# Kernel tuning notes

Measured on AMD Instinct MI355X. Metric: run time of the kernel, lower is better.

The kernel has to match this reference:

```python
import jax, jax.numpy as jnp
import numpy as np

N_NODES = 100000
N_EDGES = 3200000
F = 32          # n_node_features
L = 50          # n_node_labels
EL = 10         # n_edge_labels
K = 16          # out_dim (graph_data.num_classes)


def setup_inputs() -> dict:
    key = jax.random.key(0)
    ks = jax.random.split(key, 12)
    x = jax.random.normal(ks[0], (N_NODES, F), dtype=jnp.float32)
    node_labels = jax.random.randint(ks[1], (N_NODES,), 0, L, dtype=jnp.int32)
    edge_src = jax.random.randint(ks[2], (N_EDGES,), 0, N_NODES, dtype=jnp.int32)
    edge_dst = jax.random.randint(ks[3], (N_EDGES,), 0, N_NODES, dtype=jnp.int32)
    edge_labels = jax.random.randint(ks[4], (N_EDGES,), 0, EL, dtype=jnp.int32)
    s = 0.1
    W1 = jax.random.normal(ks[5], (L, L, EL), dtype=jnp.float32) * s
    b1 = jax.random.normal(ks[6], (L,), dtype=jnp.float32) * s
    W2 = jax.random.normal(ks[7], (L, L, EL), dtype=jnp.float32) * s
    b2 = jax.random.normal(ks[8], (L,), dtype=jnp.float32) * s
    W3 = jax.random.normal(ks[9], (L, L, EL), dtype=jnp.float32) * s
    b3 = jax.random.normal(ks[10], (L,), dtype=jnp.float32) * s
    kr1, kr2 = jax.random.split(ks[11])
    Wr = jax.random.normal(kr1, (L, F, K), dtype=jnp.float32) * s
    br = jax.random.normal(kr2, (K,), dtype=jnp.float32) * s
    return {"x": x, "W1": W1, "b1": b1, "W2": W2, "b2": b2, "W3": W3, "b3": b3,
            "Wr": Wr, "br": br, "node_labels": node_labels,
            "edge_src": edge_src, "edge_dst": edge_dst, "edge_labels": edge_labels}


def _conv(x, W, b, node_labels, edge_src, edge_dst, edge_labels):
    # weight_rule_wf: per-edge scalar weight indexed by (src label, dst label, edge label)
    w_e = W[node_labels[edge_src], node_labels[edge_dst], edge_labels]  # [E]
    msgs = w_e[:, None] * x[edge_src]                                   # [E, F]
    agg = jax.ops.segment_sum(msgs, edge_dst, num_segments=x.shape[0])  # [N, F]
    # node_label_rule bias: per-node bias indexed by node label, then Tanh
    return jnp.tanh(agg + b[node_labels][:, None])


def reference(x, W1, b1, W2, b2, W3, b3, Wr, br,
              node_labels, edge_src, edge_dst, edge_labels):
    h = _conv(x, W1, b1, node_labels, edge_src, edge_dst, edge_labels)
    h = _conv(h, W2, b2, node_labels, edge_src, edge_dst, edge_labels)
    h = _conv(h, W3, b3, node_labels, edge_src, edge_dst, edge_labels)
    # GraphResizeLayer (node_label_rule): out[k] = sum_i Wr[label_i, f, k] * h[i, f] + br[k]
    # equivalent efficient form: pre-aggregate node features by label, then contract.
    sums = jax.ops.segment_sum(h, node_labels, num_segments=Wr.shape[0])  # [L, F]
    out = jnp.tanh(jnp.einsum('lf,lfk->k', sums, Wr) + br)                # [K]
    return out
```

## Files before the change

kernel.cpp:

```cpp
#include <hip/hip_runtime.h>
#include <hip/hip_bf16.h>
#include <hip/hip_fp16.h>
#include <hip/hip_fp8.h>

#define NN 100000
#define NE 3200000
#define FF 32
#define LL 50
#define ELB 10
#define KK 16
#define NWIDX (LL * LL * ELB)

#define CH 8192
#define NBLK_P1 391
#define NBUK 391
#define CAP 9216

typedef float floatx2 __attribute__((ext_vector_type(2)));

__device__ __forceinline__ float fast_tanh(float x) {
    float e = __expf(2.0f * x);
    return 1.0f - 2.0f / (e + 1.0f);
}

__global__ __launch_bounds__(512) void p1_scatter(const int* __restrict__ esrc,
                                                  const int* __restrict__ edst,
                                                  const int* __restrict__ elab,
                                                  const float* __restrict__ x,
                                                  const float* __restrict__ W1,
                                                  const float* __restrict__ W2,
                                                  const float* __restrict__ W3,
                                                  float4* __restrict__ Wi,
                                                  unsigned char* __restrict__ labels8,
                                                  const int* __restrict__ labels,
                                                  unsigned* __restrict__ xb,
                                                  int* __restrict__ cursor,
                                                  unsigned* __restrict__ recs) {
    __shared__ int lcnt[NBUK];
    __shared__ int lofs[NBUK];
    __shared__ int lbase[NBUK];
    __shared__ int sc[512];
    __shared__ unsigned srec[CH];
    __shared__ unsigned sgad[CH];
    int tid = threadIdx.x;
    for (int i = blockIdx.x * 512 + tid; i < NN * FF / 4; i += NBLK_P1 * 512) {
        float4 v = ((const float4*)x)[i];
        __hip_fp8_e4m3 a(v.x), b(v.y), c(v.z), d(v.w);
        xb[i] = (unsigned)a.__x | ((unsigned)b.__x << 8) |
                ((unsigned)c.__x << 16) | ((unsigned)d.__x << 24);
    }
    for (int i = blockIdx.x * 512 + tid; i < NWIDX; i += NBLK_P1 * 512)
        Wi[i] = make_float4(W1[i], W2[i], W3[i], 0.f);
    for (int i = blockIdx.x * 512 + tid; i < NN; i += NBLK_P1 * 512)
        labels8[i] = (unsigned char)labels[i];
    for (int i = tid; i < NBUK; i += 512) lcnt[i] = 0;
    __syncthreads();
    long e0 = (long)blockIdx.x * CH;
    long rem = NE - e0;
    int cnt = rem < CH ? (int)rem : CH;
    int nq = cnt >> 2;
    const int4* edst4 = (const int4*)(edst + e0);
    const int4* esrc4 = (const int4*)(esrc + e0);
    const int4* elab4 = (const int4*)(elab + e0);
    for (int i = tid; i < nq; i += 512) {
        int4 d = edst4[i];
        atomicAdd(&lcnt[d.x >> 8], 1);
        atomicAdd(&lcnt[d.y >> 8], 1);
        atomicAdd(&lcnt[d.z >> 8], 1);
        atomicAdd(&lcnt[d.w >> 8], 1);
    }
    __syncthreads();
    sc[tid] = (tid < NBUK) ? lcnt[tid] : 0;
    __syncthreads();
    for (int ofs = 1; ofs < 512; ofs <<= 1) {
        int t = (tid >= ofs) ? sc[tid - ofs] : 0;
        __syncthreads();
        sc[tid] += t;
        __syncthreads();
    }
    if (tid < NBUK) {
        int c = lcnt[tid];
        lofs[tid] = sc[tid] - c;
        lbase[tid] = c ? atomicAdd(&cursor[tid], c) : 0;
        lcnt[tid] = 0;
    }
    __syncthreads();
    for (int i = tid; i < nq; i += 512) {
        int4 s4 = esrc4[i];
        int4 l4 = elab4[i];
        int4 d4 = edst4[i];
#pragma unroll
        for (int k = 0; k < 4; ++k) {
            int s  = (&s4.x)[k];
            int d  = (&d4.x)[k];
            int el = (&l4.x)[k];
            int b = d >> 8;
            int pos = atomicAdd(&lcnt[b], 1);
            int slot = lofs[b] + pos;
            srec[slot] = ((unsigned)s << 12) | ((unsigned)el << 8) | (unsigned)(d & 255);
            int rel = lbase[b] + pos;
            sgad[slot] = (rel < CAP) ? (unsigned)(b * CAP + rel) : 0xFFFFFFFFu;
        }
    }
    __syncthreads();
    for (int i = tid; i < cnt; i += 512) {
        unsigned g = sgad[i];
        if (g != 0xFFFFFFFFu)
            recs[g] = srec[i];
    }
}

__global__ __launch_bounds__(512) void p2_local(const int* __restrict__ cursor,
                                                const unsigned* __restrict__ recs,
                                                const unsigned char* __restrict__ labels8,
                                                const float4* __restrict__ Wi,
                                                unsigned long long* __restrict__ ed,
                                                int* __restrict__ gstart,
                                                int* __restrict__ gcnt) {
    __shared__ int deg[256], loff[256], lcur[256], sc[256];
    __shared__ int labd[256];
    __shared__ unsigned pk32[CAP];
    int b = blockIdx.x, tid = threadIdx.x;
    int base = b * CAP;
    int n = cursor[b];
    if (n > CAP) n = CAP;
    if (tid < 256) {
        int node = (b << 8) + tid;
        deg[tid] = 0;
        lcur[tid] = 0;
        labd[tid] = (node < NN) ? (int)labels8[node] : 0;
    }
    __syncthreads();
    for (int i = tid; i < n; i += 512)
        atomicAdd(&deg[(int)(recs[base + i] & 255)], 1);
    __syncthreads();
    if (tid < 256) sc[tid] = deg[tid];
    __syncthreads();
    for (int ofs = 1; ofs < 256; ofs <<= 1) {
        int t = (tid >= ofs && tid < 256) ? sc[tid - ofs] : 0;
        __syncthreads();
        if (tid < 256) sc[tid] += t;
        __syncthreads();
    }
    if (tid < 256) {
        loff[tid] = sc[tid] - deg[tid];
        int node = (b << 8) + tid;
        if (node < NN) { gstart[node] = base + loff[tid]; gcnt[node] = deg[tid]; }
    }
    __syncthreads();
    for (int i = tid; i < n; i += 512) {
        unsigned r = recs[base + i];
        int dl  = (int)(r & 255);
        int el  = (int)((r >> 8) & 15);
        int src = (int)(r >> 12);
        int widx = (int)labels8[src] * (LL * ELB) + labd[dl] * ELB + el;
        int ofs = atomicAdd(&lcur[dl], 1);
        pk32[loff[dl] + ofs] = ((unsigned)widx << 17) | (unsigned)src;
    }
    __syncthreads();
    for (int slot = tid; slot < n; slot += 512) {
        unsigned v = pk32[slot];
        int widx = (int)(v >> 17);
        unsigned src = v & 0x1FFFFu;
        float4 wv = Wi[widx];
        unsigned long long h1 = __half_as_ushort(__float2half(wv.x));
        unsigned long long h2 = __half_as_ushort(__float2half(wv.y));
        unsigned long long h3 = __half_as_ushort(__float2half(wv.z)) >> 1;
        ed[base + slot] = h1 | (h2 << 16) | (h3 << 32)
                        | ((unsigned long long)src << 47);
    }
}

__global__ __launch_bounds__(256) void conv_kernel(const unsigned char* __restrict__ xin,
                                                   unsigned char* __restrict__ hout,
                                                   const int* __restrict__ gstart,
                                                   const int* __restrict__ gcnt,
                                                   const unsigned long long* __restrict__ ed,
                                                   const float* __restrict__ bias,
                                                   const int* __restrict__ labels,
                                                   const int wmode) {
    __shared__ unsigned stage[2][8][64];
    int tid = threadIdx.x;
    int hw = tid >> 5, lane = tid & 31;
    int node = (blockIdx.x << 3) + hw;
    int s = gstart[node];
    int n = gcnt[node];
    float bb = bias[labels[node]];
    int eg = lane >> 3;
    int fg = (lane & 7) << 2;
    float4 acc = {0.f, 0.f, 0.f, 0.f};
    unsigned long long e_cur = ed[s + (lane < n ? lane : 0)];
    int buf = 0;
    for (int base = 0; base < n; base += 32) {
        int idx = base + lane;
        float w = 0.f;
        unsigned so = 0u;
        if (idx < n) {
            unsigned short h;
            if (wmode == 0)      h = (unsigned short)e_cur;
            else if (wmode == 1) h = (unsigned short)(e_cur >> 16);
            else                 h = (unsigned short)(((e_cur >> 32) & 0x7FFFull) << 1);
            w = __half2float(__ushort_as_half(h));
            so = (unsigned)(e_cur >> 47) << 5;
        }
        ((uint2*)&stage[buf][hw][0])[lane] = make_uint2(__float_as_uint(w), so);
        int nb = base + 32;
        if (nb < n) {
            int i2 = nb + lane;
            e_cur = ed[s + (i2 < n ? i2 : nb)];
        }
        __builtin_amdgcn_wave_barrier();
#pragma unroll
        for (int j = 0; j < 8; ++j) {
            uint2 ws = ((const uint2*)&stage[buf][hw][0])[j * 4 + eg];
            unsigned pv = *(const unsigned*)(xin + ws.y + fg);
            floatx2 lo = __builtin_amdgcn_cvt_pk_f32_fp8((int)pv, false);
            floatx2 hi = __builtin_amdgcn_cvt_pk_f32_fp8((int)pv, true);
            float we = __uint_as_float(ws.x);
            acc.x += we * lo.x;
            acc.y += we * lo.y;
            acc.z += we * hi.x;
            acc.w += we * hi.y;
        }
        buf ^= 1;
    }
    acc.x += __shfl_xor(acc.x, 8);  acc.y += __shfl_xor(acc.y, 8);
    acc.z += __shfl_xor(acc.z, 8);  acc.w += __shfl_xor(acc.w, 8);
    acc.x += __shfl_xor(acc.x, 16); acc.y += __shfl_xor(acc.y, 16);
    acc.z += __shfl_xor(acc.z, 16); acc.w += __shfl_xor(acc.w, 16);
    if (lane < 8) {
        __hip_fp8_e4m3 q0(fast_tanh(acc.x + bb));
        __hip_fp8_e4m3 q1(fast_tanh(acc.y + bb));
        __hip_fp8_e4m3 q2(fast_tanh(acc.z + bb));
        __hip_fp8_e4m3 q3(fast_tanh(acc.w + bb));
        unsigned pk = (unsigned)q0.__x | ((unsigned)q1.__x << 8) |
                      ((unsigned)q2.__x << 16) | ((unsigned)q3.__x << 24);
        ((unsigned*)(hout + ((long)node << 5)))[lane] = pk;
    }
}

__global__ __launch_bounds__(256) void lsum_kernel(const unsigned* __restrict__ h,
                                                   const int* __restrict__ labels,
                                                   float* __restrict__ sums) {
    __shared__ float ls[LL * FF];
    int tid = threadIdx.x;
    for (int i = tid; i < LL * FF; i += 256) ls[i] = 0.f;
    __syncthreads();
    for (int i = blockIdx.x * 256 + tid; i < NN * 8; i += gridDim.x * 256) {
        unsigned pv = h[i];
        int nodei = i >> 3;
        int fb = (i & 7) << 2;
        int l = labels[nodei];
        floatx2 lo = __builtin_amdgcn_cvt_pk_f32_fp8((int)pv, false);
        floatx2 hi = __builtin_amdgcn_cvt_pk_f32_fp8((int)pv, true);
        float* bp = &ls[l * FF + fb];
        atomicAdd(bp + 0, lo.x);
        atomicAdd(bp + 1, lo.y);
        atomicAdd(bp + 2, hi.x);
        atomicAdd(bp + 3, hi.y);
    }
    __syncthreads();
    for (int i = tid; i < LL * FF; i += 256) atomicAdd(&sums[i], ls[i]);
}

__global__ __launch_bounds__(256) void resize_kernel(const float* __restrict__ sums,
                                                     const float* __restrict__ Wr,
                                                     const float* __restrict__ br,
                                                     float* __restrict__ out) {
    __shared__ float red[256][KK];
    int tid = threadIdx.x;
    float acc[KK];
#pragma unroll
    for (int k = 0; k < KK; ++k) acc[k] = 0.f;
    for (int p = tid; p < LL * FF; p += 256) {
        float sv = sums[p];
#pragma unroll
        for (int k = 0; k < KK; ++k) acc[k] += sv * Wr[p * KK + k];
    }
#pragma unroll
    for (int k = 0; k < KK; ++k) red[tid][k] = acc[k];
    __syncthreads();
    for (int sft = 128; sft > 0; sft >>= 1) {
        if (tid < sft) {
#pragma unroll
            for (int k = 0; k < KK; ++k) red[tid][k] += red[tid + sft][k];
        }
        __syncthreads();
    }
    if (tid < KK) out[tid] = fast_tanh(red[0][tid] + br[tid]);
}

extern "C" void kernel_launch(void* const* d_in, const int* in_sizes, int n_in,
                              void* d_out, int out_size, void* d_ws, size_t ws_size,
                              hipStream_t stream) {
    const float* x   = (const float*)d_in[0];
    const float* W1  = (const float*)d_in[1];
    const float* b1  = (const float*)d_in[2];
    const float* W2  = (const float*)d_in[3];
    const float* b2  = (const float*)d_in[4];
    const float* W3  = (const float*)d_in[5];
    const float* b3  = (const float*)d_in[6];
    const float* Wr  = (const float*)d_in[7];
    const float* br  = (const float*)d_in[8];
    const int* labels = (const int*)d_in[9];
    const int* esrc   = (const int*)d_in[10];
    const int* edst   = (const int*)d_in[11];
    const int* elab   = (const int*)d_in[12];
    float* out = (float*)d_out;

    char* ws = (char*)d_ws;
    size_t o = 0;
    auto alloc = [&](size_t bytes) -> void* {
        void* p = ws + o;
        o += (bytes + 255) & ~(size_t)255;
        return p;
    };
    char* regionA = (char*)alloc((size_t)NBUK * CAP * sizeof(unsigned));
    unsigned* recs = (unsigned*)regionA;
    unsigned char* h1 = (unsigned char*)regionA;
    unsigned char* h2 = (unsigned char*)(regionA + (size_t)NN * FF);

    unsigned long long* ed = (unsigned long long*)alloc((size_t)NBUK * CAP * sizeof(unsigned long long));
    unsigned* xb = (unsigned*)alloc((size_t)NN * FF);
    float4* Wi   = (float4*)alloc((size_t)NWIDX * sizeof(float4));
    unsigned char* labels8 = (unsigned char*)alloc(NN);
    int* cursor = (int*)alloc(NBUK * sizeof(int));
    float* sums = (float*)alloc(LL * FF * sizeof(float));
    int* gstart = (int*)alloc(NN * sizeof(int));
    int* gcnt   = (int*)alloc(NN * sizeof(int));

    size_t msz = (size_t)((char*)sums - (char*)cursor) + LL * FF * sizeof(float);
    hipMemsetAsync(cursor, 0, msz, stream);

    p1_scatter<<<NBLK_P1, 512, 0, stream>>>(esrc, edst, elab, x, W1, W2, W3, Wi,
                                            labels8, labels, xb, cursor, recs);
    p2_local<<<NBUK, 512, 0, stream>>>(cursor, recs, labels8, Wi, ed, gstart, gcnt);

    conv_kernel<<<NN / 8, 256, 0, stream>>>((const unsigned char*)xb, h1, gstart, gcnt, ed, b1, labels, 0);
    conv_kernel<<<NN / 8, 256, 0, stream>>>(h1, h2, gstart, gcnt, ed, b2, labels, 1);
    conv_kernel<<<NN / 8, 256, 0, stream>>>(h2, h1, gstart, gcnt, ed, b3, labels, 2);

    lsum_kernel<<<256, 256, 0, stream>>>((const unsigned*)h1, labels, sums);
    resize_kernel<<<1, 256, 0, stream>>>(sums, Wr, br, out);
}
```

Measured before the change: 265.4 us.

## Split packed 64-bit edge records into three per-layer 32-bit arrays

Each conv layer now reads its own 32-bit edge stream (fp16 weight truncated to 15 bits plus a 17-bit source index) instead of one shared 64-bit record holding all three weights. This halves the edge bytes each conv pass reads. The weight table is also stored as fp16 ushort4, shrinking the gathers in p2. In exchange, p2 writes three arrays, so its total write traffic rises. All three layer weights now lose the low mantissa bit, where before only the third did, which slightly reduces precision.

```diff
diff --git a/kernel.cpp b/kernel.cpp
--- a/kernel.cpp
+++ b/kernel.cpp
@@ -30,7 +30,7 @@
                                                   const float* __restrict__ W1,
                                                   const float* __restrict__ W2,
                                                   const float* __restrict__ W3,
-                                                  float4* __restrict__ Wi,
+                                                  ushort4* __restrict__ Wi,
                                                   unsigned char* __restrict__ labels8,
                                                   const int* __restrict__ labels,
                                                   unsigned* __restrict__ xb,
@@ -49,8 +49,14 @@
         xb[i] = (unsigned)a.__x | ((unsigned)b.__x << 8) |
                 ((unsigned)c.__x << 16) | ((unsigned)d.__x << 24);
     }
-    for (int i = blockIdx.x * 512 + tid; i < NWIDX; i += NBLK_P1 * 512)
-        Wi[i] = make_float4(W1[i], W2[i], W3[i], 0.f);
+    for (int i = blockIdx.x * 512 + tid; i < NWIDX; i += NBLK_P1 * 512) {
+        ushort4 w;
+        w.x = __half_as_ushort(__float2half(W1[i]));
+        w.y = __half_as_ushort(__float2half(W2[i]));
+        w.z = __half_as_ushort(__float2half(W3[i]));
+        w.w = 0;
+        Wi[i] = w;
+    }
     for (int i = blockIdx.x * 512 + tid; i < NN; i += NBLK_P1 * 512)
         labels8[i] = (unsigned char)labels[i];
     for (int i = tid; i < NBUK; i += 512) lcnt[i] = 0;
@@ -113,8 +119,10 @@
 __global__ __launch_bounds__(512) void p2_local(const int* __restrict__ cursor,
                                                 const unsigned* __restrict__ recs,
                                                 const unsigned char* __restrict__ labels8,
-                                                const float4* __restrict__ Wi,
-                                                unsigned long long* __restrict__ ed,
+                                                const ushort4* __restrict__ Wi,
+                                                unsigned* __restrict__ ed1,
+                                                unsigned* __restrict__ ed2,
+                                                unsigned* __restrict__ ed3,
                                                 int* __restrict__ gstart,
                                                 int* __restrict__ gcnt) {
     __shared__ int deg[256], loff[256], lcur[256], sc[256];
@@ -161,13 +169,11 @@
     for (int slot = tid; slot < n; slot += 512) {
         unsigned v = pk32[slot];
         int widx = (int)(v >> 17);
-        unsigned src = v & 0x1FFFFu;
-        float4 wv = Wi[widx];
-        unsigned long long h1 = __half_as_ushort(__float2half(wv.x));
-        unsigned long long h2 = __half_as_ushort(__float2half(wv.y));
-        unsigned long long h3 = __half_as_ushort(__float2half(wv.z)) >> 1;
-        ed[base + slot] = h1 | (h2 << 16) | (h3 << 32)
-                        | ((unsigned long long)src << 47);
+        unsigned sb = (v & 0x1FFFFu) << 15;
+        ushort4 wv = Wi[widx];
+        ed1[base + slot] = (unsigned)(wv.x >> 1) | sb;
+        ed2[base + slot] = (unsigned)(wv.y >> 1) | sb;
+        ed3[base + slot] = (unsigned)(wv.z >> 1) | sb;
     }
 }
 
@@ -175,10 +181,9 @@
                                                    unsigned char* __restrict__ hout,
                                                    const int* __restrict__ gstart,
                                                    const int* __restrict__ gcnt,
-                                                   const unsigned long long* __restrict__ ed,
+                                                   const unsigned* __restrict__ ed,
                                                    const float* __restrict__ bias,
-                                                   const int* __restrict__ labels,
-                                                   const int wmode) {
+                                                   const int* __restrict__ labels) {
     __shared__ unsigned stage[2][8][64];
     int tid = threadIdx.x;
     int hw = tid >> 5, lane = tid & 31;
@@ -189,19 +194,16 @@
     int eg = lane >> 3;
     int fg = (lane & 7) << 2;
     float4 acc = {0.f, 0.f, 0.f, 0.f};
-    unsigned long long e_cur = ed[s + (lane < n ? lane : 0)];
+    unsigned e_cur = ed[s + (lane < n ? lane : 0)];
     int buf = 0;
     for (int base = 0; base < n; base += 32) {
         int idx = base + lane;
         float w = 0.f;
         unsigned so = 0u;
         if (idx < n) {
-            unsigned short h;
-            if (wmode == 0)      h = (unsigned short)e_cur;
-            else if (wmode == 1) h = (unsigned short)(e_cur >> 16);
-            else                 h = (unsigned short)(((e_cur >> 32) & 0x7FFFull) << 1);
+            unsigned short h = (unsigned short)((e_cur & 0x7FFFu) << 1);
             w = __half2float(__ushort_as_half(h));
-            so = (unsigned)(e_cur >> 47) << 5;
+            so = (e_cur >> 15) << 5;
         }
         ((uint2*)&stage[buf][hw][0])[lane] = make_uint2(__float_as_uint(w), so);
         int nb = base + 32;
@@ -320,9 +322,11 @@
     unsigned char* h1 = (unsigned char*)regionA;
     unsigned char* h2 = (unsigned char*)(regionA + (size_t)NN * FF);
 
-    unsigned long long* ed = (unsigned long long*)alloc((size_t)NBUK * CAP * sizeof(unsigned long long));
+    unsigned* ed1 = (unsigned*)alloc((size_t)NBUK * CAP * sizeof(unsigned));
+    unsigned* ed2 = (unsigned*)alloc((size_t)NBUK * CAP * sizeof(unsigned));
+    unsigned* ed3 = (unsigned*)alloc((size_t)NBUK * CAP * sizeof(unsigned));
     unsigned* xb = (unsigned*)alloc((size_t)NN * FF);
-    float4* Wi   = (float4*)alloc((size_t)NWIDX * sizeof(float4));
+    ushort4* Wi  = (ushort4*)alloc((size_t)NWIDX * sizeof(ushort4));
     unsigned char* labels8 = (unsigned char*)alloc(NN);
     int* cursor = (int*)alloc(NBUK * sizeof(int));
     float* sums = (float*)alloc(LL * FF * sizeof(float));
@@ -334,11 +338,11 @@
 
     p1_scatter<<<NBLK_P1, 512, 0, stream>>>(esrc, edst, elab, x, W1, W2, W3, Wi,
                                             labels8, labels, xb, cursor, recs);
-    p2_local<<<NBUK, 512, 0, stream>>>(cursor, recs, labels8, Wi, ed, gstart, gcnt);
-
-    conv_kernel<<<NN / 8, 256, 0, stream>>>((const unsigned char*)xb, h1, gstart, gcnt, ed, b1, labels, 0);
-    conv_kernel<<<NN / 8, 256, 0, stream>>>(h1, h2, gstart, gcnt, ed, b2, labels, 1);
-    conv_kernel<<<NN / 8, 256, 0, stream>>>(h2, h1, gstart, gcnt, ed, b3, labels, 2);
+    p2_local<<<NBUK, 512, 0, stream>>>(cursor, recs, labels8, Wi, ed1, ed2, ed3, gstart, gcnt);
+
+    conv_kernel<<<NN / 8, 256, 0, stream>>>((const unsigned char*)xb, h1, gstart, gcnt, ed1, b1, labels);
+    conv_kernel<<<NN / 8, 256, 0, stream>>>(h1, h2, gstart, gcnt, ed2, b2, labels);
+    conv_kernel<<<NN / 8, 256, 0, stream>>>(h2, h1, gstart, gcnt, ed3, b3, labels);
 
     lsum_kernel<<<256, 256, 0, stream>>>((const unsigned*)h1, labels, sums);
     resize_kernel<<<1, 256, 0, stream>>>(sums, Wr, br, out);
```

Result: no change. 260.9 us (-1.7%).
